# Kernel optimization log

Measured on AMD Instinct MI355X. Metric: run time of the kernel, lower is better.

Reference implementation:

```python
import jax, jax.numpy as jnp
import numpy as np

B, S, F, H = 2, 2048, 1024, 16
D = F // H  # 64 head dim


def setup_inputs() -> dict:
    key = jax.random.key(0)
    ks = jax.random.split(key, 11)
    std = 1.0 / np.sqrt(F)
    inp = {
        "q": jax.random.normal(ks[0], (B, S, F), dtype=jnp.float32),
        "k": jax.random.normal(ks[1], (B, S, F), dtype=jnp.float32),
        "v": jax.random.normal(ks[2], (B, S, F), dtype=jnp.float32),
        "wq_w": jax.random.normal(ks[3], (F, F), dtype=jnp.float32) * std,
        "wq_b": jnp.zeros((F,), dtype=jnp.float32),
        "wk_w": jax.random.normal(ks[4], (F, F), dtype=jnp.float32) * std,
        "wk_b": jnp.zeros((F,), dtype=jnp.float32),
        "wv_w": jax.random.normal(ks[5], (F, F), dtype=jnp.float32) * std,
        "wv_b": jnp.zeros((F,), dtype=jnp.float32),
        "fc_w": jax.random.normal(ks[6], (F, F), dtype=jnp.float32) * std,
        "fc_b": jnp.zeros((F,), dtype=jnp.float32),
    }
    return inp


def _split_heads(x):
    # [B, S, F] -> [B, H, S, D]
    return x.reshape(B, S, H, D).transpose(0, 2, 1, 3)


def reference(q, k, v, wq_w, wq_b, wk_w, wk_b, wv_w, wv_b, fc_w, fc_b):
    # Linear projections (torch Linear: x @ W^T + b)
    qh = _split_heads(q @ wq_w.T + wq_b)
    kh = _split_heads(k @ wk_w.T + wk_b)
    vh = _split_heads(v @ wv_w.T + wv_b)
    # scaled dot product attention, explicit [B,H,S,S] scores as in source
    scale = 1.0 / np.sqrt(D)
    scores = jnp.einsum("bhqd,bhkd->bhqk", qh, kh) * scale
    attn = jax.nn.softmax(scores, axis=-1)
    ctx = jnp.einsum("bhqk,bhkd->bhqd", attn, vh)
    # merge heads: [B,H,S,D] -> [B,S,F]
    concat = ctx.transpose(0, 2, 1, 3).reshape(B, S, F)
    out = concat @ fc_w.T + fc_b
    out = jax.nn.relu(out)  # activation=F.relu_ default
    return (out, attn)
```

## Files before the change

### kernel.cpp

```cpp
#include <hip/hip_runtime.h>
#include <stdint.h>

#define DEV __device__ __forceinline__

using f32x4  = __attribute__((ext_vector_type(4))) float;
using bf16x8 = __attribute__((ext_vector_type(8))) __bf16;
using bf16x4 = __attribute__((ext_vector_type(4))) __bf16;

static constexpr int SEQ  = 2048;
static constexpr int FEA  = 1024;
static constexpr int NHEAD = 16;
static constexpr int MROWS = 4096;
static constexpr float QK_SCALE = 0.18033688011112042f;

DEV f32x4 mfma16(bf16x8 a, bf16x8 b, f32x4 c) {
  return __builtin_amdgcn_mfma_f32_16x16x32_bf16(a, b, c, 0, 0, 0);
}

DEV void gload16(const void* g, void* l) {
  __builtin_amdgcn_global_load_lds((__attribute__((address_space(1))) void*)g,
                                   (__attribute__((address_space(3))) void*)l,
                                   16, 0, 0);
}

#define FENCE_VMCNT(n) asm volatile("s_waitcnt vmcnt(" #n ")" ::: "memory")
#define FENCE_LGKM0()  asm volatile("s_waitcnt lgkmcnt(0)" ::: "memory")

struct ConvSeg { const float* src; __bf16* dst; int n4; float scale; };
struct ConvArgs { ConvSeg seg[7]; };

__global__ __launch_bounds__(256) void convert_k(ConvArgs a) {
  const ConvSeg sg = a.seg[blockIdx.y];
  const int stride = gridDim.x * blockDim.x;
  for (int i = blockIdx.x * blockDim.x + threadIdx.x; i < sg.n4; i += stride) {
    const f32x4 v = *(const f32x4*)(sg.src + (size_t)i * 4);
    bf16x4 o = {(__bf16)(v[0] * sg.scale), (__bf16)(v[1] * sg.scale),
                (__bf16)(v[2] * sg.scale), (__bf16)(v[3] * sg.scale)};
    *(bf16x4*)(sg.dst + (size_t)i * 4) = o;
  }
}

DEV void gemm_core64(const __bf16* __restrict__ A, const __bf16* __restrict__ Bt,
                     char* lds, int row0, int col0, int tid, f32x4 (&acc)[4][4]) {
  char* Alds = lds;
  char* Blds = lds + 16384;
  constexpr int K = 1024;
  const int lane = tid & 63;
  const int w    = tid >> 6;
  const int ci   = lane & 15;
  const int g    = lane >> 4;
  const int wr   = w >> 1, wc = w & 1;

  const __bf16* gA[4]; const __bf16* gB[4];
  char* lA[4]; char* lB[4];
#pragma unroll
  for (int j = 0; j < 4; ++j) {
    const int c = tid + 256 * j;
    const int r = c >> 3, s = c & 7;
    const int gsw = (s ^ (r & 7)) * 8;
    gA[j] = A  + (size_t)(row0 + r) * K + gsw;
    gB[j] = Bt + (size_t)(col0 + r) * K + gsw;
    lA[j] = Alds + c * 16;
    lB[j] = Blds + c * 16;
  }
  const int rsw = (ci & 7) << 4;

  for (int k0 = 0; k0 < K; k0 += 64) {
    __syncthreads();
#pragma unroll
    for (int j = 0; j < 4; ++j) {
      gload16(gA[j] + k0, lA[j]);
      gload16(gB[j] + k0, lB[j]);
    }
    __syncthreads();
#pragma unroll
    for (int kk = 0; kk < 2; ++kk) {
      bf16x8 af[4], bfr[4];
#pragma unroll
      for (int m = 0; m < 4; ++m)
        af[m] = *(const bf16x8*)(Alds + (wr * 64 + m * 16 + ci) * 128 +
                                 ((kk * 64 + g * 16) ^ rsw));
#pragma unroll
      for (int n = 0; n < 4; ++n)
        bfr[n] = *(const bf16x8*)(Blds + (wc * 64 + n * 16 + ci) * 128 +
                                  ((kk * 64 + g * 16) ^ rsw));
#pragma unroll
      for (int m = 0; m < 4; ++m)
#pragma unroll
        for (int n = 0; n < 4; ++n)
          acc[m][n] = mfma16(af[m], bfr[n], acc[m][n]);
    }
  }
}

struct QkvArgs {
  const __bf16* A[3];
  const __bf16* Bt[3];
  const float*  bias[3];
  float         bscale[3];
  __bf16*       out[3];
};

__global__ __launch_bounds__(256) void gemm_qkv(QkvArgs args) {
  __shared__ __align__(16) char lds[32768];
  const int z = blockIdx.z;
  const int tid = threadIdx.x;
  const int row0 = blockIdx.x * 128;
  const int col0 = blockIdx.y * 128;
  f32x4 acc[4][4] = {};
  gemm_core64(args.A[z], args.Bt[z], lds, row0, col0, tid, acc);

  const int lane = tid & 63;
  const int ci = lane & 15, g = lane >> 4;
  const int w = tid >> 6;
  const int wr = w >> 1, wc = w & 1;
  const float* bias = args.bias[z];
  const float bscale = args.bscale[z];
  __bf16* outp = args.out[z];
  const bool vt = (z == 2);
#pragma unroll
  for (int m = 0; m < 4; ++m)
#pragma unroll
    for (int n = 0; n < 4; ++n)
#pragma unroll
      for (int r = 0; r < 4; ++r) {
        const int gr = row0 + wr * 64 + m * 16 + 4 * g + r;
        const int gc = col0 + wc * 64 + n * 16 + ci;
        const float vv = acc[m][n][r] + bias[gc] * bscale;
        const int b = gr >> 11, s = gr & (SEQ - 1);
        const int h = gc >> 6,  d = gc & 63;
        if (!vt)
          outp[(((size_t)b * NHEAD + h) * SEQ + s) * 64 + d] = (__bf16)vv;
        else
          outp[(((size_t)b * NHEAD + h) * 64 + d) * SEQ + s] = (__bf16)vv;
      }
}

__global__ __launch_bounds__(256) void gemm_fc(const __bf16* __restrict__ A,
                                               const __bf16* __restrict__ Bt,
                                               const float* __restrict__ bias,
                                               float* __restrict__ outp) {
  __shared__ __align__(16) char lds[32768];
  const int tid = threadIdx.x;
  const int row0 = blockIdx.x * 128;
  const int col0 = blockIdx.y * 128;
  f32x4 acc[4][4] = {};
  gemm_core64(A, Bt, lds, row0, col0, tid, acc);

  const int lane = tid & 63;
  const int ci = lane & 15, g = lane >> 4;
  const int w = tid >> 6;
  const int wr = w >> 1, wc = w & 1;
#pragma unroll
  for (int m = 0; m < 4; ++m)
#pragma unroll
    for (int n = 0; n < 4; ++n)
#pragma unroll
      for (int r = 0; r < 4; ++r) {
        const int gr = row0 + wr * 64 + m * 16 + 4 * g + r;
        const int gc = col0 + wc * 64 + n * 16 + ci;
        const float vv = fmaxf(acc[m][n][r] + bias[gc], 0.0f);
        __builtin_nontemporal_store(vv, &outp[(size_t)gr * FEA + gc]);
      }
}

static constexpr int QBLK = 32;
static constexpr int KVB  = 128;
static constexpr int NT   = SEQ / KVB;

__global__ __launch_bounds__(512, 4) void attn_fused(const __bf16* __restrict__ Qh,
                                                     const __bf16* __restrict__ Kh,
                                                     const __bf16* __restrict__ VhT,
                                                     float* __restrict__ attn_out,
                                                     __bf16* __restrict__ Cbuf) {
  __shared__ __align__(16) char smem[65536];
  __shared__ float rs_lds[8][16];
  __shared__ float linv_lds[QBLK];
  float* pvf = (float*)smem;

  const int tid  = threadIdx.x;
  const int lane = tid & 63;
  const int w    = tid >> 6;
  const int ci   = lane & 15;
  const int g    = lane >> 4;
  const int qg   = w >> 2;
  const int kg   = w & 3;

  const int id   = blockIdx.x;
  const int xcd  = id & 7;
  const int idx  = id >> 3;
  const int bh   = xcd * 4 + (idx >> 6);
  const int qblk = idx & 63;

  const __bf16* Qp   = Qh + ((size_t)bh * SEQ + qblk * QBLK) * 64;
  const char*   Kbyt = (const char*)(Kh  + (size_t)bh * SEQ * 64);
  const char*   Vbyt = (const char*)(VhT + (size_t)bh * 64 * SEQ);

  const int cA = tid, cB = tid + 512;
  const int kgoffA = ((cA >> 3) * 128) + (((cA & 7) ^ ((cA >> 3) & 7)) * 16);
  const int kgoffB = ((cB >> 3) * 128) + (((cB & 7) ^ ((cB >> 3) & 7)) * 16);
  const int vdA = cA >> 4, vdB = cB >> 4;
  const int vgoffA = vdA * (SEQ * 2) + (((cA & 15) ^ (vdA & 7)) * 16);
  const int vgoffB = vdB * (SEQ * 2) + (((cB & 15) ^ (vdB & 7)) * 16);

#define STAGE_K(t, boff) { gload16(Kbyt + (size_t)(t) * 16384 + kgoffA, smem + (boff) + cA * 16); \
                           gload16(Kbyt + (size_t)(t) * 16384 + kgoffB, smem + (boff) + cB * 16); }
#define STAGE_V(t, boff) { gload16(Vbyt + (size_t)(t) * 256 + vgoffA, smem + 16384 + (boff) + cA * 16); \
                           gload16(Vbyt + (size_t)(t) * 256 + vgoffB, smem + 16384 + (boff) + cB * 16); }

  const bf16x8 q0 = *(const bf16x8*)(Qp + (qg * 16 + ci) * 64 + 8 * g);
  const bf16x8 q1 = *(const bf16x8*)(Qp + (qg * 16 + ci) * 64 + 32 + 8 * g);

  const int kswz  = (ci & 7) << 4;
  const int krow0 = kg * 4096 + ci * 128;

  float rs = 0.f;
  STAGE_K(0, 0);
  STAGE_K(1, 16384);
  for (int p = 0; p < NT / 2; ++p) {
    const int base = (p & 1) << 15;
    __builtin_amdgcn_s_barrier();
    if (p < NT / 2 - 1) {
      STAGE_K(2 * p + 2, base ^ 32768);
      STAGE_K(2 * p + 3, (base ^ 32768) + 16384);
      FENCE_VMCNT(4);
    } else {
      FENCE_VMCNT(0);
    }
#pragma unroll
    for (int hb = 0; hb < 2; ++hb) {
      const char* kt = smem + base + hb * 16384 + krow0;
#pragma unroll
      for (int s = 0; s < 2; ++s) {
        const bf16x8 k0 = *(const bf16x8*)(kt + s * 2048 + ((16 * g) ^ kswz));
        const bf16x8 k1 = *(const bf16x8*)(kt + s * 2048 + ((64 + 16 * g) ^ kswz));
        f32x4 sf = {0.f, 0.f, 0.f, 0.f};
        sf = mfma16(k0, q0, sf);
        sf = mfma16(k1, q1, sf);
#pragma unroll
        for (int r = 0; r < 4; ++r) rs += __builtin_amdgcn_exp2f(sf[r]);
      }
    }
    FENCE_LGKM0();
  }
  rs += __shfl_xor(rs, 16);
  rs += __shfl_xor(rs, 32);
  if (lane < 16) rs_lds[w][lane] = rs;
  __syncthreads();
  if (tid < QBLK) {
    const int qg2 = tid >> 4;
    float tsum = 0.f;
#pragma unroll
    for (int kk = 0; kk < 4; ++kk) tsum += rs_lds[qg2 * 4 + kk][tid & 15];
    linv_lds[tid] = -__log2f(tsum);
  }
  __syncthreads();
  const float linv = linv_lds[qg * 16 + ci];

  f32x4 apv[4] = {};
  float* orow = attn_out + ((size_t)bh * SEQ + qblk * QBLK + qg * 16 + ci) * SEQ +
                kg * 32 + 4 * g;

  STAGE_K(0, 0);
  STAGE_V(0, 0);
  for (int t = 0; t < NT; ++t) {
    const int coff = (t & 1) << 15;
    __builtin_amdgcn_s_barrier();
    if (t < NT - 1) {
      STAGE_K(t + 1, coff ^ 32768);
      STAGE_V(t + 1, coff ^ 32768);
      if (t == 0) FENCE_VMCNT(4);
      else        FENCE_VMCNT(6);
    } else {
      FENCE_VMCNT(2);
    }

    f32x4 e[2];
#pragma unroll
    for (int s = 0; s < 2; ++s) {
      const char* kt = smem + coff + krow0 + s * 2048;
      const bf16x8 k0 = *(const bf16x8*)(kt + ((16 * g) ^ kswz));
      const bf16x8 k1 = *(const bf16x8*)(kt + ((64 + 16 * g) ^ kswz));
      f32x4 sf = {0.f, 0.f, 0.f, 0.f};
      sf = mfma16(k0, q0, sf);
      sf = mfma16(k1, q1, sf);
#pragma unroll
      for (int r = 0; r < 4; ++r) e[s][r] = __builtin_amdgcn_exp2f(sf[r] + linv);
      __builtin_nontemporal_store(e[s], (f32x4*)(orow + t * 128 + s * 16));
    }
    const bf16x8 pa = {(__bf16)e[0][0], (__bf16)e[0][1], (__bf16)e[0][2], (__bf16)e[0][3],
                       (__bf16)e[1][0], (__bf16)e[1][1], (__bf16)e[1][2], (__bf16)e[1][3]};
    const int inr0 = (64 * kg + 8 * g) ^ kswz;
    const int inr1 = (64 * kg + 32 + 8 * g) ^ kswz;
#pragma unroll
    for (int dt = 0; dt < 4; ++dt) {
      const char* vrow = smem + 16384 + coff + (dt * 16 + ci) * 256;
      const bf16x4 v0 = *(const bf16x4*)(vrow + inr0);
      const bf16x4 v1 = *(const bf16x4*)(vrow + inr1);
      const bf16x8 vb = {v0[0], v0[1], v0[2], v0[3], v1[0], v1[1], v1[2], v1[3]};
      apv[dt] = mfma16(pa, vb, apv[dt]);
    }
    FENCE_LGKM0();
  }
  __syncthreads();

  {
    const int base = (qg * 4 + kg) * 16;
#pragma unroll
    for (int dt = 0; dt < 4; ++dt)
#pragma unroll
      for (int r = 0; r < 4; ++r)
        pvf[(base + 4 * g + r) * 68 + dt * 16 + ci] = apv[dt][r];
  }
  __syncthreads();
  {
    const int qq  = tid >> 4;
    const int d0  = (tid & 15) * 4;
    const int qg2 = qq >> 4, row = qq & 15;
    f32x4 s = {0.f, 0.f, 0.f, 0.f};
#pragma unroll
    for (int kk = 0; kk < 4; ++kk)
      s += *(const f32x4*)&pvf[((qg2 * 4 + kk) * 16 + row) * 68 + d0];
    const int b = bh >> 4, h = bh & 15;
    const bf16x4 o = {(__bf16)s[0], (__bf16)s[1], (__bf16)s[2], (__bf16)s[3]};
    *(bf16x4*)&Cbuf[((size_t)b * SEQ + qblk * QBLK + qq) * FEA + h * 64 + d0] = o;
  }
#undef STAGE_K
#undef STAGE_V
}

extern "C" void kernel_launch(void* const* d_in, const int* in_sizes, int n_in,
                              void* d_out, int out_size, void* d_ws, size_t ws_size,
                              hipStream_t stream) {
  const float* q    = (const float*)d_in[0];
  const float* k    = (const float*)d_in[1];
  const float* v    = (const float*)d_in[2];
  const float* wq_w = (const float*)d_in[3];
  const float* wq_b = (const float*)d_in[4];
  const float* wk_w = (const float*)d_in[5];
  const float* wk_b = (const float*)d_in[6];
  const float* wv_w = (const float*)d_in[7];
  const float* wv_b = (const float*)d_in[8];
  const float* fc_w = (const float*)d_in[9];
  const float* fc_b = (const float*)d_in[10];

  float* out0 = (float*)d_out;
  float* attn = out0 + (size_t)MROWS * FEA;

  __bf16* Xq = (__bf16*)attn;
  __bf16* Xk = Xq + (size_t)MROWS * FEA;
  __bf16* Xv = Xk + (size_t)MROWS * FEA;
  __bf16* Wq = Xv + (size_t)MROWS * FEA;
  __bf16* Wk = Wq + (size_t)FEA * FEA;
  __bf16* Wv = Wk + (size_t)FEA * FEA;

  __bf16* Qh  = (__bf16*)d_ws;
  __bf16* Kh  = Qh  + (size_t)MROWS * FEA;
  __bf16* VhT = Kh  + (size_t)MROWS * FEA;
  __bf16* Cb  = VhT + (size_t)MROWS * FEA;
  __bf16* Wfc = Cb  + (size_t)MROWS * FEA;

  ConvArgs ca;
  ca.seg[0] = {q,    Xq,  (MROWS * FEA) / 4, 1.0f};
  ca.seg[1] = {k,    Xk,  (MROWS * FEA) / 4, 1.0f};
  ca.seg[2] = {v,    Xv,  (MROWS * FEA) / 4, 1.0f};
  ca.seg[3] = {wq_w, Wq,  (FEA * FEA) / 4,   QK_SCALE};
  ca.seg[4] = {wk_w, Wk,  (FEA * FEA) / 4,   1.0f};
  ca.seg[5] = {wv_w, Wv,  (FEA * FEA) / 4,   1.0f};
  ca.seg[6] = {fc_w, Wfc, (FEA * FEA) / 4,   1.0f};
  convert_k<<<dim3(512, 7), 256, 0, stream>>>(ca);

  QkvArgs qa;
  qa.A[0] = Xq; qa.Bt[0] = Wq; qa.bias[0] = wq_b; qa.bscale[0] = QK_SCALE; qa.out[0] = Qh;
  qa.A[1] = Xk; qa.Bt[1] = Wk; qa.bias[1] = wk_b; qa.bscale[1] = 1.0f;     qa.out[1] = Kh;
  qa.A[2] = Xv; qa.Bt[2] = Wv; qa.bias[2] = wv_b; qa.bscale[2] = 1.0f;     qa.out[2] = VhT;
  gemm_qkv<<<dim3(MROWS / 128, FEA / 128, 3), 256, 0, stream>>>(qa);

  attn_fused<<<dim3((SEQ / QBLK) * NHEAD * 2), 512, 0, stream>>>(Qh, Kh, VhT, attn, Cb);

  gemm_fc<<<dim3(MROWS / 128, FEA / 128), 256, 0, stream>>>(Cb, Wfc, fc_b, out0);
}
```

Before: 233.8 us.

## Process four query tiles per block, fusing next tile's row-sum pass into current pass

Each attention block now handles four consecutive 32-row query tiles instead of one, and the grid shrinks from 2048 to 512 blocks. While computing the normalized probabilities and PV product for tile i, it also computes the exp row sums for tile i+1 from the same K tiles in LDS. This removes the separate K-only normalization pass for all but the first tile, cutting K reloads and redundant QK work. The cost is fewer blocks, which may reduce occupancy and load balance, plus more registers and serialized tiles per block.

```diff
diff --git a/kernel.cpp b/kernel.cpp
--- a/kernel.cpp
+++ b/kernel.cpp
@@ -165,6 +165,7 @@
 }
 
 static constexpr int QBLK = 32;
+static constexpr int GQT  = 4;
 static constexpr int KVB  = 128;
 static constexpr int NT   = SEQ / KVB;
 
@@ -176,7 +177,7 @@
   __shared__ __align__(16) char smem[65536];
   __shared__ float rs_lds[8][16];
   __shared__ float linv_lds[QBLK];
-  float* pvf = (float*)smem;
+  float* pvf = (float*)(smem + 32768);
 
   const int tid  = threadIdx.x;
   const int lane = tid & 63;
@@ -189,12 +190,12 @@
   const int id   = blockIdx.x;
   const int xcd  = id & 7;
   const int idx  = id >> 3;
-  const int bh   = xcd * 4 + (idx >> 6);
-  const int qblk = idx & 63;
-
-  const __bf16* Qp   = Qh + ((size_t)bh * SEQ + qblk * QBLK) * 64;
-  const char*   Kbyt = (const char*)(Kh  + (size_t)bh * SEQ * 64);
-  const char*   Vbyt = (const char*)(VhT + (size_t)bh * 64 * SEQ);
+  const int bh   = xcd * 4 + (idx >> 4);
+  const int qgrp = idx & 15;
+
+  const __bf16* Qbase = Qh + ((size_t)bh * SEQ + (size_t)qgrp * (QBLK * GQT)) * 64;
+  const char*   Kbyt  = (const char*)(Kh  + (size_t)bh * SEQ * 64);
+  const char*   Vbyt  = (const char*)(VhT + (size_t)bh * 64 * SEQ);
 
   const int cA = tid, cB = tid + 512;
   const int kgoffA = ((cA >> 3) * 128) + (((cA & 7) ^ ((cA >> 3) & 7)) * 16);
@@ -208,11 +209,15 @@
 #define STAGE_V(t, boff) { gload16(Vbyt + (size_t)(t) * 256 + vgoffA, smem + 16384 + (boff) + cA * 16); \
                            gload16(Vbyt + (size_t)(t) * 256 + vgoffB, smem + 16384 + (boff) + cB * 16); }
 
-  const bf16x8 q0 = *(const bf16x8*)(Qp + (qg * 16 + ci) * 64 + 8 * g);
-  const bf16x8 q1 = *(const bf16x8*)(Qp + (qg * 16 + ci) * 64 + 32 + 8 * g);
-
   const int kswz  = (ci & 7) << 4;
   const int krow0 = kg * 4096 + ci * 128;
+
+  bf16x8 cq0, cq1;
+  {
+    const __bf16* qp = Qbase + (qg * 16 + ci) * 64;
+    cq0 = *(const bf16x8*)(qp + 8 * g);
+    cq1 = *(const bf16x8*)(qp + 32 + 8 * g);
+  }
 
   float rs = 0.f;
   STAGE_K(0, 0);
@@ -235,8 +240,8 @@
         const bf16x8 k0 = *(const bf16x8*)(kt + s * 2048 + ((16 * g) ^ kswz));
         const bf16x8 k1 = *(const bf16x8*)(kt + s * 2048 + ((64 + 16 * g) ^ kswz));
         f32x4 sf = {0.f, 0.f, 0.f, 0.f};
-        sf = mfma16(k0, q0, sf);
-        sf = mfma16(k1, q1, sf);
+        sf = mfma16(k0, cq0, sf);
+        sf = mfma16(k1, cq1, sf);
 #pragma unroll
         for (int r = 0; r < 4; ++r) rs += __builtin_amdgcn_exp2f(sf[r]);
       }
@@ -249,81 +254,114 @@
   __syncthreads();
   if (tid < QBLK) {
     const int qg2 = tid >> 4;
-    float tsum = 0.f;
-#pragma unroll
-    for (int kk = 0; kk < 4; ++kk) tsum += rs_lds[qg2 * 4 + kk][tid & 15];
-    linv_lds[tid] = -__log2f(tsum);
+    float ts = 0.f;
+#pragma unroll
+    for (int kk = 0; kk < 4; ++kk) ts += rs_lds[qg2 * 4 + kk][tid & 15];
+    linv_lds[tid] = -__log2f(ts);
   }
   __syncthreads();
-  const float linv = linv_lds[qg * 16 + ci];
-
-  f32x4 apv[4] = {};
-  float* orow = attn_out + ((size_t)bh * SEQ + qblk * QBLK + qg * 16 + ci) * SEQ +
-                kg * 32 + 4 * g;
-
-  STAGE_K(0, 0);
-  STAGE_V(0, 0);
-  for (int t = 0; t < NT; ++t) {
-    const int coff = (t & 1) << 15;
-    __builtin_amdgcn_s_barrier();
-    if (t < NT - 1) {
-      STAGE_K(t + 1, coff ^ 32768);
-      STAGE_V(t + 1, coff ^ 32768);
-      if (t == 0) FENCE_VMCNT(4);
-      else        FENCE_VMCNT(6);
-    } else {
-      FENCE_VMCNT(2);
-    }
-
-    f32x4 e[2];
-#pragma unroll
-    for (int s = 0; s < 2; ++s) {
-      const char* kt = smem + coff + krow0 + s * 2048;
-      const bf16x8 k0 = *(const bf16x8*)(kt + ((16 * g) ^ kswz));
-      const bf16x8 k1 = *(const bf16x8*)(kt + ((64 + 16 * g) ^ kswz));
-      f32x4 sf = {0.f, 0.f, 0.f, 0.f};
-      sf = mfma16(k0, q0, sf);
-      sf = mfma16(k1, q1, sf);
-#pragma unroll
-      for (int r = 0; r < 4; ++r) e[s][r] = __builtin_amdgcn_exp2f(sf[r] + linv);
-      __builtin_nontemporal_store(e[s], (f32x4*)(orow + t * 128 + s * 16));
-    }
-    const bf16x8 pa = {(__bf16)e[0][0], (__bf16)e[0][1], (__bf16)e[0][2], (__bf16)e[0][3],
-                       (__bf16)e[1][0], (__bf16)e[1][1], (__bf16)e[1][2], (__bf16)e[1][3]};
-    const int inr0 = (64 * kg + 8 * g) ^ kswz;
-    const int inr1 = (64 * kg + 32 + 8 * g) ^ kswz;
-#pragma unroll
-    for (int dt = 0; dt < 4; ++dt) {
-      const char* vrow = smem + 16384 + coff + (dt * 16 + ci) * 256;
-      const bf16x4 v0 = *(const bf16x4*)(vrow + inr0);
-      const bf16x4 v1 = *(const bf16x4*)(vrow + inr1);
-      const bf16x8 vb = {v0[0], v0[1], v0[2], v0[3], v1[0], v1[1], v1[2], v1[3]};
-      apv[dt] = mfma16(pa, vb, apv[dt]);
-    }
+
+  for (int i = 0; i < GQT; ++i) {
+    const bool more = (i + 1 < GQT);
+    bf16x8 nq0 = {}, nq1 = {};
+    if (more) {
+      const __bf16* qp = Qbase + ((i + 1) * QBLK + qg * 16 + ci) * 64;
+      nq0 = *(const bf16x8*)(qp + 8 * g);
+      nq1 = *(const bf16x8*)(qp + 32 + 8 * g);
+    }
+    const float linv = linv_lds[qg * 16 + ci];
+    float* orow = attn_out + ((size_t)bh * SEQ + (size_t)(qgrp * GQT + i) * QBLK +
+                              qg * 16 + ci) * SEQ + kg * 32 + 4 * g;
+    f32x4 apv[4] = {};
+    float nrs = 0.f;
+
+    STAGE_K(0, 0);
+    STAGE_V(0, 0);
+    for (int t = 0; t < NT; ++t) {
+      const int coff = (t & 1) << 15;
+      __builtin_amdgcn_s_barrier();
+      if (t < NT - 1) {
+        STAGE_K(t + 1, coff ^ 32768);
+        STAGE_V(t + 1, coff ^ 32768);
+        if (t == 0) FENCE_VMCNT(4);
+        else        FENCE_VMCNT(6);
+      } else {
+        FENCE_VMCNT(2);
+      }
+
+      f32x4 e[2];
+#pragma unroll
+      for (int s = 0; s < 2; ++s) {
+        const char* kt = smem + coff + krow0 + s * 2048;
+        const bf16x8 k0 = *(const bf16x8*)(kt + ((16 * g) ^ kswz));
+        const bf16x8 k1 = *(const bf16x8*)(kt + ((64 + 16 * g) ^ kswz));
+        f32x4 sf = {0.f, 0.f, 0.f, 0.f};
+        sf = mfma16(k0, cq0, sf);
+        sf = mfma16(k1, cq1, sf);
+        if (more) {
+          f32x4 nsf = {0.f, 0.f, 0.f, 0.f};
+          nsf = mfma16(k0, nq0, nsf);
+          nsf = mfma16(k1, nq1, nsf);
+#pragma unroll
+          for (int r = 0; r < 4; ++r) nrs += __builtin_amdgcn_exp2f(nsf[r]);
+        }
+#pragma unroll
+        for (int r = 0; r < 4; ++r) e[s][r] = __builtin_amdgcn_exp2f(sf[r] + linv);
+        __builtin_nontemporal_store(e[s], (f32x4*)(orow + t * 128 + s * 16));
+      }
+      const bf16x8 pa = {(__bf16)e[0][0], (__bf16)e[0][1], (__bf16)e[0][2], (__bf16)e[0][3],
+                         (__bf16)e[1][0], (__bf16)e[1][1], (__bf16)e[1][2], (__bf16)e[1][3]};
+      const int inr0 = (64 * kg + 8 * g) ^ kswz;
+      const int inr1 = (64 * kg + 32 + 8 * g) ^ kswz;
+#pragma unroll
+      for (int dt = 0; dt < 4; ++dt) {
+        const char* vrow = smem + 16384 + coff + (dt * 16 + ci) * 256;
+        const bf16x4 v0 = *(const bf16x4*)(vrow + inr0);
+        const bf16x4 v1 = *(const bf16x4*)(vrow + inr1);
+        const bf16x8 vb = {v0[0], v0[1], v0[2], v0[3], v1[0], v1[1], v1[2], v1[3]};
+        apv[dt] = mfma16(pa, vb, apv[dt]);
+      }
+      FENCE_LGKM0();
+    }
+
+    __syncthreads();
+    {
+      const int basew = (qg * 4 + kg) * 16;
+#pragma unroll
+      for (int dt = 0; dt < 4; ++dt)
+#pragma unroll
+        for (int r = 0; r < 4; ++r)
+          pvf[(basew + 4 * g + r) * 64 + dt * 16 + ci] = apv[dt][r];
+    }
+    if (more) {
+      nrs += __shfl_xor(nrs, 16);
+      nrs += __shfl_xor(nrs, 32);
+      if (lane < 16) rs_lds[w][lane] = nrs;
+    }
+    __syncthreads();
+    {
+      const int qq  = tid >> 4;
+      const int d0  = (tid & 15) * 4;
+      const int qg2 = qq >> 4, row = qq & 15;
+      f32x4 ss = {0.f, 0.f, 0.f, 0.f};
+#pragma unroll
+      for (int kk = 0; kk < 4; ++kk)
+        ss += *(const f32x4*)&pvf[((qg2 * 4 + kk) * 16 + row) * 64 + d0];
+      const int b = bh >> 4, h = bh & 15;
+      const int srow = (qgrp * GQT + i) * QBLK + qq;
+      const bf16x4 o = {(__bf16)ss[0], (__bf16)ss[1], (__bf16)ss[2], (__bf16)ss[3]};
+      *(bf16x4*)&Cbuf[((size_t)b * SEQ + srow) * FEA + h * 64 + d0] = o;
+    }
+    if (more && tid < QBLK) {
+      const int qg2 = tid >> 4;
+      float ts = 0.f;
+#pragma unroll
+      for (int kk = 0; kk < 4; ++kk) ts += rs_lds[qg2 * 4 + kk][tid & 15];
+      linv_lds[tid] = -__log2f(ts);
+    }
+    cq0 = nq0; cq1 = nq1;
     FENCE_LGKM0();
-  }
-  __syncthreads();
-
-  {
-    const int base = (qg * 4 + kg) * 16;
-#pragma unroll
-    for (int dt = 0; dt < 4; ++dt)
-#pragma unroll
-      for (int r = 0; r < 4; ++r)
-        pvf[(base + 4 * g + r) * 68 + dt * 16 + ci] = apv[dt][r];
-  }
-  __syncthreads();
-  {
-    const int qq  = tid >> 4;
-    const int d0  = (tid & 15) * 4;
-    const int qg2 = qq >> 4, row = qq & 15;
-    f32x4 s = {0.f, 0.f, 0.f, 0.f};
-#pragma unroll
-    for (int kk = 0; kk < 4; ++kk)
-      s += *(const f32x4*)&pvf[((qg2 * 4 + kk) * 16 + row) * 68 + d0];
-    const int b = bh >> 4, h = bh & 15;
-    const bf16x4 o = {(__bf16)s[0], (__bf16)s[1], (__bf16)s[2], (__bf16)s[3]};
-    *(bf16x4*)&Cbuf[((size_t)b * SEQ + qblk * QBLK + qq) * FEA + h * 64 + d0] = o;
+    __syncthreads();
   }
 #undef STAGE_K
 #undef STAGE_V
@@ -376,7 +414,7 @@
   qa.A[2] = Xv; qa.Bt[2] = Wv; qa.bias[2] = wv_b; qa.bscale[2] = 1.0f;     qa.out[2] = VhT;
   gemm_qkv<<<dim3(MROWS / 128, FEA / 128, 3), 256, 0, stream>>>(qa);
 
-  attn_fused<<<dim3((SEQ / QBLK) * NHEAD * 2), 512, 0, stream>>>(Qh, Kh, VhT, attn, Cb);
+  attn_fused<<<dim3(512), 512, 0, stream>>>(Qh, Kh, VhT, attn, Cb);
 
   gemm_fc<<<dim3(MROWS / 128, FEA / 128), 256, 0, stream>>>(Cb, Wfc, fc_b, out0);
 }
```

New measurement: 223.7 us. 1.05x faster.
